# Kernel tuning notes

Hardware: AMD Instinct MI355X
Metric: run time of the kernel (lower is better)

## Reference

```python
import jax, jax.numpy as jnp
import numpy as np

HIDDEN = 1024
ARC = 500
BATCH = 16
SEQ = 512


def setup_inputs() -> dict:
    key = jax.random.key(0)
    ks = jax.random.split(key, 12)
    s_h = 1.0 / np.sqrt(HIDDEN)
    s_a = 1.0 / np.sqrt(ARC)
    return {
        "hidden_states": jax.random.normal(ks[0], (BATCH, SEQ, HIDDEN), dtype=jnp.float32),
        # head MLP: Linear(hidden->arc), ReLU, (Dropout eval=identity), Linear(arc->arc)
        "w1h": jax.random.uniform(ks[1], (ARC, HIDDEN), jnp.float32, -s_h, s_h),
        "b1h": jax.random.uniform(ks[2], (ARC,), jnp.float32, -s_h, s_h),
        "w2h": jax.random.uniform(ks[3], (ARC, ARC), jnp.float32, -s_a, s_a),
        "b2h": jax.random.uniform(ks[4], (ARC,), jnp.float32, -s_a, s_a),
        # dep MLP
        "w1d": jax.random.uniform(ks[5], (ARC, HIDDEN), jnp.float32, -s_h, s_h),
        "b1d": jax.random.uniform(ks[6], (ARC,), jnp.float32, -s_h, s_h),
        "w2d": jax.random.uniform(ks[7], (ARC, ARC), jnp.float32, -s_a, s_a),
        "b2d": jax.random.uniform(ks[8], (ARC,), jnp.float32, -s_a, s_a),
        # nn.Bilinear(arc, arc, 1, bias=True): weight [1, arc, arc], bias [1]
        "Wb": jax.random.uniform(ks[9], (ARC, ARC), jnp.float32, -s_a, s_a),
        "bb": jax.random.uniform(ks[10], (1,), jnp.float32, -s_a, s_a),
    }


def reference(hidden_states, w1h, b1h, w2h, b2h, w1d, b1d, w2d, b2d, Wb, bb):
    # MLPs (dropout is identity at inference)
    head = jnp.maximum(hidden_states @ w1h.T + b1h, 0.0) @ w2h.T + b2h  # [B,S,A]
    dep = jnp.maximum(hidden_states @ w1d.T + b1d, 0.0) @ w2d.T + b2d  # [B,S,A]
    # seq_len <= 512 already; chunked bilinear == two GEMMs:
    # scores[b,i,j] = head[b,i] @ Wb @ dep[b,j] + bb
    headW = head @ Wb  # [B,S,A]
    arc_scores = jnp.einsum("bia,bja->bij", headW, dep) + bb[0]  # [B,S,S]
    return arc_scores
```

## Files before the change

kernel.cpp:

```cpp
#include <hip/hip_runtime.h>
#include <hip/hip_bf16.h>


#define HIDDEN 1024
#define ARC 500
#define AP 512
#define ROWS 8192

typedef __attribute__((ext_vector_type(4))) float f32x4;
typedef __attribute__((ext_vector_type(8))) short short8;

static __device__ __forceinline__ ushort f2bf(float f) {
  union { float f; unsigned u; } v; v.f = f;
  unsigned r = v.u + 0x7fffu + ((v.u >> 16) & 1u);
  return (ushort)(r >> 16);
}

__global__ void k_prep_all(const float* __restrict__ w1h, const float* __restrict__ b1h,
                           const float* __restrict__ w1d, const float* __restrict__ b1d,
                           const float* __restrict__ w2h, const float* __restrict__ b2h,
                           const float* __restrict__ w2d, const float* __restrict__ b2d,
                           const float* __restrict__ Wb, const float4* __restrict__ hs,
                           ushort* __restrict__ W1, ushort* __restrict__ WbT,
                           ushort* __restrict__ w2hT, ushort* __restrict__ W2,
                           float* __restrict__ b1c, ushort* __restrict__ hs_bf) {
  const int bid = blockIdx.x;
  const int tid = threadIdx.x;
  if (bid < 4096) {
    int idx = bid * 256 + tid;
    int n = idx >> 10, k = idx & 1023;
    float v = 0.f;
    if (n < ARC) v = w1h[(size_t)n * HIDDEN + k];
    else if (n >= AP && n < AP + ARC) v = w1d[(size_t)(n - AP) * HIDDEN + k];
    W1[idx] = f2bf(v);
  } else if (bid < 5120) {
    int idx = (bid - 4096) * 256 + tid;
    int a = idx >> 9, j = idx & 511;
    float v = (a < ARC && j < ARC) ? Wb[(size_t)j * ARC + a] : 0.f;
    WbT[idx] = f2bf(v);
  } else if (bid < 6144) {
    int idx = (bid - 5120) * 256 + tid;
    int k = idx >> 9, j = idx & 511;
    float v = 0.f;
    if (j < ARC) {
      if (k < ARC) v = w2h[(size_t)j * ARC + k];
      else if (k == 511) v = b2h[j];
    }
    w2hT[idx] = f2bf(v);
  } else if (bid < 7168) {
    int idx = (bid - 6144) * 256 + tid;
    int n = idx >> 9, k = idx & 511;
    float v = 0.f;
    if (n < ARC) {
      if (k < ARC) v = w2d[(size_t)n * ARC + k];
      else if (k == 511) v = b2d[n];
    }
    W2[idx] = f2bf(v);
  } else if (bid < 7172) {
    int i = (bid - 7168) * 256 + tid;
    float v = 0.f;
    if (i < ARC) v = b1h[i];
    else if (i == 511 || i == 1023) v = 1.f;
    else if (i >= AP && i < AP + ARC) v = b1d[i - AP];
    b1c[i] = v;
  } else {
    const int n4 = ROWS * HIDDEN / 4;
    int i = (bid - 7172) * 256 + tid;
    for (; i < n4; i += 2048 * 256) {
      float4 v = hs[i];
      ushort4 o;
      o.x = f2bf(v.x); o.y = f2bf(v.y); o.z = f2bf(v.z); o.w = f2bf(v.w);
      *(ushort4*)(hs_bf + (size_t)i * 4) = o;
    }
  }
}

template <int BN>
__device__ __forceinline__ void gemm_body(
    const ushort* __restrict__ A, const ushort* __restrict__ B,
    const float* __restrict__ bias, int bias_mode,
    void* __restrict__ C, int out_bf16, int relu,
    int lda, int ldb, int ldc, int K, int tm, int tn, ushort* lds) {
  constexpr int WC = BN / 2;
  constexpr int NFR = WC / 16;
  ushort* As0 = lds;
  ushort* As1 = lds + 4096;
  ushort* Bs0 = lds + 8192;
  ushort* Bs1 = lds + 8192 + BN * 32;

  const int t = threadIdx.x;
  const int w = t >> 6;
  const int l = t & 63;
  const int wr = w >> 1, wc = w & 1;

  f32x4 acc[4][NFR];
#pragma unroll
  for (int m = 0; m < 4; ++m)
#pragma unroll
    for (int n = 0; n < NFR; ++n) acc[m][n] = f32x4{0.f, 0.f, 0.f, 0.f};

  const int srow = w * 16 + (l >> 2);
  const int scol = (((l & 3) ^ ((l >> 3) & 3))) * 8;
  const ushort* ag = A + (size_t)(tm + srow) * lda + scol;
  const ushort* bg = B + (size_t)(tn + srow) * ldb + scol;
  const int lofs = w * 512;

  const int fr = l & 15, fh = l >> 4;
  const int swz = (fr >> 1) & 3;
  const int fAo = (wr * 64 + fr) * 32 + (fh ^ swz) * 8;
  const int fBo = (wc * WC + fr) * 32 + (fh ^ swz) * 8;

  auto stage = [&](int kt, ushort* lA, ushort* lB) {
#pragma unroll
    for (int c = 0; c < 2; ++c)
      __builtin_amdgcn_global_load_lds(
          (const __attribute__((address_space(1))) void*)(ag + (size_t)c * 64 * lda + kt),
          (__attribute__((address_space(3))) void*)(lA + lofs + c * 2048), 16, 0, 0);
#pragma unroll
    for (int c = 0; c < BN / 64; ++c)
      __builtin_amdgcn_global_load_lds(
          (const __attribute__((address_space(1))) void*)(bg + (size_t)c * 64 * ldb + kt),
          (__attribute__((address_space(3))) void*)(lB + lofs + c * 2048), 16, 0, 0);
  };
  auto compute = [&](const ushort* As, const ushort* Bs) {
    short8 af[4], bf[NFR];
#pragma unroll
    for (int m = 0; m < 4; ++m) af[m] = *(const short8*)(As + fAo + m * 16 * 32);
#pragma unroll
    for (int n = 0; n < NFR; ++n) bf[n] = *(const short8*)(Bs + fBo + n * 16 * 32);
#pragma unroll
    for (int m = 0; m < 4; ++m)
#pragma unroll
      for (int n = 0; n < NFR; ++n)
        acc[m][n] = __builtin_amdgcn_mfma_f32_16x16x32_bf16(af[m], bf[n], acc[m][n], 0, 0, 0);
  };

  const int nt = K >> 5;
  stage(0, As0, Bs0);
  for (int ti = 0; ti < nt; ti += 2) {
    __syncthreads();
    if (ti + 1 < nt) stage((ti + 1) << 5, As1, Bs1);
    compute(As0, Bs0);
    __syncthreads();
    if (ti + 2 < nt) stage((ti + 2) << 5, As0, Bs0);
    compute(As1, Bs1);
  }

  const int cr = fh * 4;
  const float bscal = (bias_mode == 2) ? bias[0] : 0.f;
#pragma unroll
  for (int m = 0; m < 4; ++m) {
#pragma unroll
    for (int n = 0; n < NFR; ++n) {
      const int col = tn + wc * WC + n * 16 + fr;
      const float bv = (bias_mode == 1) ? bias[col] : bscal;
#pragma unroll
      for (int j = 0; j < 4; ++j) {
        const int row = tm + wr * 64 + m * 16 + cr + j;
        float v = acc[m][n][j] + bv;
        if (relu) v = fmaxf(v, 0.f);
        if (out_bf16)
          ((ushort*)C)[(size_t)row * ldc + col] = f2bf(v);
        else
          ((float*)C)[(size_t)row * ldc + col] = v;
      }
    }
  }
}

__global__ __launch_bounds__(256)
void k_g1mt(const ushort* __restrict__ hs_bf, const ushort* __restrict__ W1,
            const float* __restrict__ b1c, ushort* __restrict__ t1,
            const ushort* __restrict__ WbT, const ushort* __restrict__ w2hT,
            ushort* __restrict__ MTb) {
  __shared__ ushort lds[16384];
  const int flat = blockIdx.y * 8 + blockIdx.x;
  const int f2 = (flat & 7) * 66 + (flat >> 3);
  const int by = f2 >> 3, bx = f2 & 7;
  if (by < 64) {
    gemm_body<128>(hs_bf, W1, b1c, 1, t1, 1, 1,
                   HIDDEN, HIDDEN, 1024, HIDDEN, by * 128, bx * 128, lds);
  } else {
    const int idx = (by - 64) * 8 + bx;
    gemm_body<128>(WbT, w2hT, nullptr, 0, MTb, 1, 0,
                   AP, AP, AP, AP, (idx >> 2) * 128, (idx & 3) * 128, lds);
  }
}

template <int BN>
__global__ __launch_bounds__(256)
void k_gemm_rt(const ushort* __restrict__ A, const ushort* __restrict__ B,
               const float* __restrict__ bias, int bias_mode,
               void* __restrict__ C, int out_bf16, int relu,
               int lda, int ldb, int ldc, int K,
               long aBS, long bBS, long cBS) {
  __shared__ ushort lds[8192 + BN * 64];
  const int gx = gridDim.x, gy = gridDim.y;
  const int gxy = gx * gy;
  const int nwg = gxy * gridDim.z;
  const int flat = (blockIdx.z * gy + blockIdx.y) * gx + blockIdx.x;
  const int q = nwg >> 3;
  const int f2 = (flat & 7) * q + (flat >> 3);
  const int bz = f2 / gxy;
  const int rm = f2 - bz * gxy;
  const int by = rm / gx;
  const int bx = rm - by * gx;

  const ushort* Az = A + (size_t)aBS * bz;
  const ushort* Bz = B + (size_t)bBS * bz;
  void* Cz = out_bf16 ? (void*)((ushort*)C + (size_t)cBS * bz)
                      : (void*)((float*)C + (size_t)cBS * bz);
  gemm_body<BN>(Az, Bz, bias, bias_mode, Cz, out_bf16, relu,
                lda, ldb, ldc, K, by * 128, bx * BN, lds);
}

extern "C" void kernel_launch(void* const* d_in, const int* in_sizes, int n_in,
                              void* d_out, int out_size, void* d_ws, size_t ws_size,
                              hipStream_t stream) {
  const float* hs  = (const float*)d_in[0];
  const float* w1h = (const float*)d_in[1];
  const float* b1h = (const float*)d_in[2];
  const float* w2h = (const float*)d_in[3];
  const float* b2h = (const float*)d_in[4];
  const float* w1d = (const float*)d_in[5];
  const float* b1d = (const float*)d_in[6];
  const float* w2d = (const float*)d_in[7];
  const float* b2d = (const float*)d_in[8];
  const float* Wb  = (const float*)d_in[9];
  const float* bb  = (const float*)d_in[10];

  char* ws = (char*)d_ws;
  ushort* hs_bf = (ushort*)(ws + 0);
  ushort* W1    = (ushort*)(ws + 16777216);
  ushort* WbT   = (ushort*)(ws + 18874368);
  ushort* w2hT  = (ushort*)(ws + 19398656);
  ushort* MT    = (ushort*)(ws + 19922944);
  ushort* W2    = (ushort*)(ws + 20447232);
  ushort* t1    = (ushort*)(ws + 20971520);
  ushort* hw    = (ushort*)(ws + 37748736);
  float*  b1c   = (float*)(ws + 54525952);
  float*  out   = (float*)d_out;

  k_prep_all<<<9220, 256, 0, stream>>>(w1h, b1h, w1d, b1d, w2h, b2h, w2d, b2d,
                                       Wb, (const float4*)hs,
                                       W1, WbT, w2hT, W2, b1c, hs_bf);

  k_g1mt<<<dim3(8, 66), 256, 0, stream>>>(hs_bf, W1, b1c, t1, WbT, w2hT, MT);

  k_gemm_rt<128><<<dim3(4, 64, 2), 256, 0, stream>>>(
      t1, MT, nullptr, 0, hw, 1, 0, 1024, AP, AP, AP,
      AP, (long)AP * AP, (long)ROWS * AP);

  k_gemm_rt<64><<<dim3(8, 4, 16), 256, 0, stream>>>(
      hw, hw + (size_t)ROWS * AP, bb, 2, out, 0, 0, AP, AP, 512, AP,
      (long)512 * AP, (long)512 * AP, (long)512 * 512);
}
```

Measured before the change: 171.8 us.

## Switch GEMM mainloop to triple-buffered LDS pipeline with single barrier per k-step

Replaces the double-buffered A/B LDS staging with a three-stage ring buffer. Two tiles are prefetched ahead, and each iteration waits on a partial vmcnt before a single barrier instead of two syncthreads. This keeps more global-to-LDS loads in flight and halves the barrier count, aiming to hide memory latency behind the MFMA work. It costs more LDS per block (48KB for BN=128), which may reduce occupancy, and it relies on exact vmcnt counts matching the number of loads issued per stage.

Result: faster. 163.3 us (-4.9%).

```diff
diff --git a/kernel.cpp b/kernel.cpp
--- a/kernel.cpp
+++ b/kernel.cpp
@@ -83,10 +83,7 @@
     int lda, int ldb, int ldc, int K, int tm, int tn, ushort* lds) {
   constexpr int WC = BN / 2;
   constexpr int NFR = WC / 16;
-  ushort* As0 = lds;
-  ushort* As1 = lds + 4096;
-  ushort* Bs0 = lds + 8192;
-  ushort* Bs1 = lds + 8192 + BN * 32;
+  constexpr int BUFSZ = 4096 + BN * 32;
 
   const int t = threadIdx.x;
   const int w = t >> 6;
@@ -110,24 +107,24 @@
   const int fAo = (wr * 64 + fr) * 32 + (fh ^ swz) * 8;
   const int fBo = (wc * WC + fr) * 32 + (fh ^ swz) * 8;
 
-  auto stage = [&](int kt, ushort* lA, ushort* lB) {
+  auto stage = [&](int kt, ushort* buf) {
 #pragma unroll
     for (int c = 0; c < 2; ++c)
       __builtin_amdgcn_global_load_lds(
           (const __attribute__((address_space(1))) void*)(ag + (size_t)c * 64 * lda + kt),
-          (__attribute__((address_space(3))) void*)(lA + lofs + c * 2048), 16, 0, 0);
+          (__attribute__((address_space(3))) void*)(buf + lofs + c * 2048), 16, 0, 0);
 #pragma unroll
     for (int c = 0; c < BN / 64; ++c)
       __builtin_amdgcn_global_load_lds(
           (const __attribute__((address_space(1))) void*)(bg + (size_t)c * 64 * ldb + kt),
-          (__attribute__((address_space(3))) void*)(lB + lofs + c * 2048), 16, 0, 0);
+          (__attribute__((address_space(3))) void*)(buf + 4096 + lofs + c * 2048), 16, 0, 0);
   };
-  auto compute = [&](const ushort* As, const ushort* Bs) {
+  auto compute = [&](const ushort* buf) {
     short8 af[4], bf[NFR];
 #pragma unroll
-    for (int m = 0; m < 4; ++m) af[m] = *(const short8*)(As + fAo + m * 16 * 32);
-#pragma unroll
-    for (int n = 0; n < NFR; ++n) bf[n] = *(const short8*)(Bs + fBo + n * 16 * 32);
+    for (int m = 0; m < 4; ++m) af[m] = *(const short8*)(buf + fAo + m * 16 * 32);
+#pragma unroll
+    for (int n = 0; n < NFR; ++n) bf[n] = *(const short8*)(buf + 4096 + fBo + n * 16 * 32);
 #pragma unroll
     for (int m = 0; m < 4; ++m)
 #pragma unroll
@@ -136,14 +133,22 @@
   };
 
   const int nt = K >> 5;
-  stage(0, As0, Bs0);
-  for (int ti = 0; ti < nt; ti += 2) {
-    __syncthreads();
-    if (ti + 1 < nt) stage((ti + 1) << 5, As1, Bs1);
-    compute(As0, Bs0);
-    __syncthreads();
-    if (ti + 2 < nt) stage((ti + 2) << 5, As0, Bs0);
-    compute(As1, Bs1);
+  stage(0, lds);
+  stage(32, lds + BUFSZ);
+  int cs = 0, ps = 2;
+  for (int ti = 0; ti < nt; ++ti) {
+    if (ti + 1 < nt) {
+      if constexpr (BN == 128) asm volatile("s_waitcnt vmcnt(4)" ::: "memory");
+      else                     asm volatile("s_waitcnt vmcnt(3)" ::: "memory");
+    } else {
+      asm volatile("s_waitcnt vmcnt(0)" ::: "memory");
+    }
+    __builtin_amdgcn_s_barrier();
+    __builtin_amdgcn_sched_barrier(0);
+    if (ti + 2 < nt) stage((ti + 2) << 5, lds + ps * BUFSZ);
+    compute(lds + cs * BUFSZ);
+    cs = (cs == 2) ? 0 : cs + 1;
+    ps = (ps == 2) ? 0 : ps + 1;
   }
 
   const int cr = fh * 4;
@@ -173,7 +178,7 @@
             const float* __restrict__ b1c, ushort* __restrict__ t1,
             const ushort* __restrict__ WbT, const ushort* __restrict__ w2hT,
             ushort* __restrict__ MTb) {
-  __shared__ ushort lds[16384];
+  __shared__ ushort lds[3 * 8192];
   const int flat = blockIdx.y * 8 + blockIdx.x;
   const int f2 = (flat & 7) * 66 + (flat >> 3);
   const int by = f2 >> 3, bx = f2 & 7;
@@ -194,7 +199,7 @@
                void* __restrict__ C, int out_bf16, int relu,
                int lda, int ldb, int ldc, int K,
                long aBS, long bBS, long cBS) {
-  __shared__ ushort lds[8192 + BN * 64];
+  __shared__ ushort lds[3 * (4096 + BN * 32)];
   const int gx = gridDim.x, gy = gridDim.y;
   const int gxy = gx * gy;
   const int nwg = gxy * gridDim.z;
```
